# Optimization experiments

Hardware: AMD Instinct MI355X
Metric: run time of the kernel (lower is better)

## Reference

```python
import jax, jax.numpy as jnp
import numpy as np

N = 100000
E = 1600000
F_IN = 128
HID = 64


def setup_inputs() -> dict:
    key = jax.random.key(0)
    ks = jax.random.split(key, 8)
    x = jax.random.normal(ks[0], (N, F_IN), dtype=jnp.float32)
    edge_index = jax.random.randint(ks[1], (2, E), 0, N, dtype=jnp.int32)
    # GCNConv params: weight [in, out] (glorot-ish scale), bias [out]
    W1 = jax.random.normal(ks[2], (F_IN, HID), dtype=jnp.float32) / np.sqrt(F_IN)
    b1 = jnp.zeros((HID,), dtype=jnp.float32)
    W2 = jax.random.normal(ks[3], (HID, HID), dtype=jnp.float32) / np.sqrt(HID)
    b2 = jnp.zeros((HID,), dtype=jnp.float32)
    Wc = jax.random.normal(ks[4], (HID, 1), dtype=jnp.float32) / np.sqrt(HID)
    bc = jnp.zeros((1,), dtype=jnp.float32)
    return {"x": x, "edge_index": edge_index, "W1": W1, "b1": b1,
            "W2": W2, "b2": b2, "Wc": Wc, "bc": bc}


def _gcn_conv(x, src, dst, W, b):
    # PyG GCNConv: h = x @ W, then symmetric-normalized aggregation over
    # edges with self-loops: out[d] = sum_e deg^-1/2[s] deg^-1/2[d] h[s] + b
    n = x.shape[0]
    h = x @ W                                            # [N, out]
    deg = jax.ops.segment_sum(jnp.ones_like(dst, dtype=h.dtype), dst,
                              num_segments=n)            # in-degree incl. self-loops
    dinv = jnp.where(deg > 0, jax.lax.rsqrt(deg), 0.0)   # [N]
    norm = dinv[src] * dinv[dst]                         # [E+N]
    msg = h[src] * norm[:, None]                         # gather + scale
    out = jax.ops.segment_sum(msg, dst, num_segments=n)  # scatter-add
    return out + b


def reference(x, edge_index, W1, b1, W2, b2, Wc, bc):
    n = x.shape[0]
    loop = jnp.arange(n, dtype=edge_index.dtype)
    src = jnp.concatenate([edge_index[0], loop])  # add self-loops
    dst = jnp.concatenate([edge_index[1], loop])
    h = jax.nn.relu(_gcn_conv(x, src, dst, W1, b1))  # dropout in eval mode = identity
    h = jax.nn.relu(_gcn_conv(h, src, dst, W2, b2))
    return (h @ Wc + bc).squeeze(-1)  # [N]
```

## Files before the change

### kernel.cpp

```cpp
#include <hip/hip_runtime.h>


#define FIN 128
#define HIDDEN 64
#define BUCK_SH 7
#define BUCK_MASK 127
#define NBUCK 782
#define CAP 2432
#define EPB 2048

typedef __attribute__((ext_vector_type(8))) short bf16x8;
typedef __attribute__((ext_vector_type(4))) float f32x4;

__device__ __forceinline__ unsigned f2bf_pair(float a, float b) {
    unsigned ua = __float_as_uint(a);
    unsigned ub = __float_as_uint(b);
    ua = (ua + 0x7FFFu + ((ua >> 16) & 1u)) >> 16;
    ub = (ub + 0x7FFFu + ((ub >> 16) & 1u)) & 0xFFFF0000u;
    return ua | ub;
}
__device__ __forceinline__ unsigned short f2bf1(float a) {
    unsigned u = __float_as_uint(a);
    return (unsigned short)((u + 0x7FFFu + ((u >> 16) & 1u)) >> 16);
}
#define BF_LO(u) __uint_as_float((u) << 16)
#define BF_HI(u) __uint_as_float((u) & 0xFFFF0000u)

__global__ __launch_bounds__(256) void k_prep(const float* __restrict__ w1,
                                              const float* __restrict__ w2,
                                              unsigned short* __restrict__ w1t,
                                              unsigned short* __restrict__ w2t,
                                              int* __restrict__ bcursor) {
    int t = blockIdx.x * 256 + threadIdx.x;
    if (t < NBUCK) bcursor[t] = 0;
    for (int i = t; i < 64 * FIN; i += 16384) {
        int ch = i >> 7, k = i & 127;
        w1t[i] = f2bf1(w1[k * 64 + ch]);
    }
    if (t < 64 * 64) {
        int ch = t >> 6, k = t & 63;
        w2t[t] = f2bf1(w2[k * 64 + ch]);
    }
}

__global__ __launch_bounds__(256) void k_scatter_mfma1(const int* __restrict__ src,
                                                       const int* __restrict__ dst,
                                                       int* __restrict__ bcursor,
                                                       int* __restrict__ pairs, int e,
                                                       const float4* __restrict__ x4,
                                                       const unsigned short* __restrict__ w1t,
                                                       uint2* __restrict__ hsb,
                                                       int n, int nsc, int ngm) {
    __shared__ int sbuf[4352];
    int tid = threadIdx.x;
    int bid = blockIdx.x;
    bool is_sc = (bid & 1) == 0;
    int id = bid >> 1;
    if (is_sc) {
        if (id >= nsc) return;
        int* h      = sbuf;
        int* base_s = sbuf + NBUCK;
        int* cur    = sbuf + 2 * NBUCK;
        int dloc[EPB / 256];
        for (int i = tid; i < NBUCK; i += 256) { h[i] = 0; cur[i] = 0; }
        __syncthreads();
        int start = id * EPB;
#pragma unroll
        for (int i = 0; i < EPB / 256; i++) {
            int idx = start + tid + i * 256;
            int d = (idx < e) ? dst[idx] : -1;
            dloc[i] = d;
            if (d >= 0) atomicAdd(&h[d >> BUCK_SH], 1);
        }
        __syncthreads();
        for (int i = tid; i < NBUCK; i += 256)
            if (h[i] > 0) base_s[i] = atomicAdd(&bcursor[i], h[i]);
        __syncthreads();
#pragma unroll
        for (int i = 0; i < EPB / 256; i++) {
            int idx = start + tid + i * 256;
            int d = dloc[i];
            if (d >= 0) {
                int b = d >> BUCK_SH;
                int pos = base_s[b] + atomicAdd(&cur[b], 1);
                if (pos < CAP) pairs[b * CAP + pos] = (src[idx] << BUCK_SH) | (d & BUCK_MASK);
            }
        }
        return;
    }
    if (id >= ngm) return;
    unsigned short* sW = (unsigned short*)sbuf;
    {
        int ch = tid >> 2, k0 = (tid & 3) * 32;
        const uint4* g = (const uint4*)(w1t + ch * 128 + k0);
        uint4* dsd = (uint4*)(sW + ch * 136 + k0);
        uint4 a = g[0], b = g[1], c = g[2], d = g[3];
        dsd[0] = a; dsd[1] = b; dsd[2] = c; dsd[3] = d;
    }
    __syncthreads();
    int lane = tid & 63, wave = tid >> 6;
    int quad = lane >> 4, nl = lane & 15;
    const bf16x8* sW8 = (const bf16x8*)sW;
    int node0g = id * 128;
#pragma unroll
    for (int hf = 0; hf < 2; hf++) {
        int node = node0g + hf * 64 + wave * 16 + nl;
        int ic = min(node, n - 1);
        const float4* px = x4 + (size_t)ic * 32 + quad * 2;
        bf16x8 bfr[4];
#pragma unroll
        for (int kc = 0; kc < 4; kc++) {
            float4 p = px[kc * 8];
            float4 q = px[kc * 8 + 1];
            union { unsigned u[4]; bf16x8 v; } t;
            t.u[0] = f2bf_pair(p.x, p.y); t.u[1] = f2bf_pair(p.z, p.w);
            t.u[2] = f2bf_pair(q.x, q.y); t.u[3] = f2bf_pair(q.z, q.w);
            bfr[kc] = t.v;
        }
        f32x4 a0 = {0.f, 0.f, 0.f, 0.f}, a1 = a0, a2 = a0, a3 = a0;
#pragma unroll
        for (int kc = 0; kc < 4; kc++) {
            int ko = kc * 4 + quad;
            bf16x8 w0  = sW8[(nl +  0) * 17 + ko];
            bf16x8 w1f = sW8[(nl + 16) * 17 + ko];
            bf16x8 w2f = sW8[(nl + 32) * 17 + ko];
            bf16x8 w3f = sW8[(nl + 48) * 17 + ko];
            a0 = __builtin_amdgcn_mfma_f32_16x16x32_bf16(w0,  bfr[kc], a0, 0, 0, 0);
            a1 = __builtin_amdgcn_mfma_f32_16x16x32_bf16(w1f, bfr[kc], a1, 0, 0, 0);
            a2 = __builtin_amdgcn_mfma_f32_16x16x32_bf16(w2f, bfr[kc], a2, 0, 0, 0);
            a3 = __builtin_amdgcn_mfma_f32_16x16x32_bf16(w3f, bfr[kc], a3, 0, 0, 0);
        }
        if (node < n) {
            uint2* o = hsb + (size_t)node * 16 + quad;
            o[0]  = make_uint2(f2bf_pair(a0.x, a0.y), f2bf_pair(a0.z, a0.w));
            o[4]  = make_uint2(f2bf_pair(a1.x, a1.y), f2bf_pair(a1.z, a1.w));
            o[8]  = make_uint2(f2bf_pair(a2.x, a2.y), f2bf_pair(a2.z, a2.w));
            o[12] = make_uint2(f2bf_pair(a3.x, a3.y), f2bf_pair(a3.z, a3.w));
        }
    }
}

__global__ __launch_bounds__(256) void k_count(const int* __restrict__ pairs,
                                               const int* __restrict__ bcursor,
                                               float* __restrict__ dinv, int n) {
    __shared__ int cnt[128];
    int tid = threadIdx.x, b = blockIdx.x;
    if (tid < 128) cnt[tid] = 0;
    __syncthreads();
    int c = min(bcursor[b], CAP);
    const int* pb = pairs + b * CAP;
    for (int i = tid; i < c; i += 256) atomicAdd(&cnt[pb[i] & BUCK_MASK], 1);
    __syncthreads();
    int node = (b << BUCK_SH) + tid;
    if (tid < 128 && node < n) dinv[node] = rsqrtf((float)cnt[tid] + 1.0f);
}

__global__ __launch_bounds__(256) void k_agg1_gemm2(const int* __restrict__ pairs,
                                                    const int* __restrict__ bcursor,
                                                    const float* __restrict__ dinv,
                                                    const uint4* __restrict__ hsb4,
                                                    const float4* __restrict__ b1_4,
                                                    const unsigned short* __restrict__ w2t,
                                                    uint2* __restrict__ hsb2, int n) {
    __shared__ int csr_l[CAP];
    __shared__ unsigned short sW[64 * 72];
    __shared__ float sV[32 * 68];
    __shared__ int cnt[128], off_s[128], wsum[128];
    int tid = threadIdx.x, b = blockIdx.x;
    int node0 = b << BUCK_SH;
    if (tid < 128) {
        int ch = tid >> 1, k0 = (tid & 1) * 32;
        const uint4* g = (const uint4*)(w2t + ch * 64 + k0);
        uint4* dsd = (uint4*)(sW + ch * 72 + k0);
        uint4 a = g[0], bb = g[1], c = g[2], d = g[3];
        dsd[0] = a; dsd[1] = bb; dsd[2] = c; dsd[3] = d;
    } else {
        cnt[tid - 128] = 0;
    }
    __syncthreads();
    int c = min(bcursor[b], CAP);
    const int* pb = pairs + b * CAP;
    for (int i = tid; i < c; i += 256) atomicAdd(&cnt[pb[i] & BUCK_MASK], 1);
    __syncthreads();
    if (tid < 128) wsum[tid] = cnt[tid];
    __syncthreads();
    for (int o = 1; o < 128; o <<= 1) {
        int x = 0;
        if (tid < 128 && tid >= o) x = wsum[tid - o];
        __syncthreads();
        if (tid < 128 && tid >= o) wsum[tid] += x;
        __syncthreads();
    }
    if (tid < 128) { off_s[tid] = wsum[tid] - cnt[tid]; cnt[tid] = 0; }
    __syncthreads();
    for (int i = tid; i < c; i += 256) {
        int p = pb[i];
        int l = p & BUCK_MASK;
        int pos = off_s[l] + atomicAdd(&cnt[l], 1);
        csr_l[pos] = p >> BUCK_SH;
    }
    __syncthreads();
    int nloc = tid >> 3, cq = tid & 7;
    int lane = tid & 63, wave = tid >> 6;
    int quad = lane >> 4, nl = lane & 15;
    const bf16x8* sW8 = (const bf16x8*)sW;
#pragma unroll 1
    for (int ck = 0; ck < 4; ck++) {
        int loc = ck * 32 + nloc;
        int node = node0 + loc;
        int dg = cnt[loc], st = off_s[loc];
        float sd = rsqrtf((float)dg + 1.0f);
        float4 accA = make_float4(0.f, 0.f, 0.f, 0.f), accB = accA;
        if (node < n) {
            int end = st + dg;
            int nr = (dg + 3) >> 2;
            for (int r = 0; r < nr; r++) {
                int base = st + (r << 2);
                int e0 = base, e1 = base + 1, e2 = base + 2, e3 = base + 3;
                int s0 = csr_l[min(e0, end - 1)];
                int s1 = csr_l[min(e1, end - 1)];
                int s2 = csr_l[min(e2, end - 1)];
                int s3 = csr_l[min(e3, end - 1)];
                float m0 = (e0 < end) ? dinv[s0] : 0.f;
                float m1 = (e1 < end) ? dinv[s1] : 0.f;
                float m2 = (e2 < end) ? dinv[s2] : 0.f;
                float m3 = (e3 < end) ? dinv[s3] : 0.f;
                uint4 g0 = hsb4[(size_t)s0 * 8 + cq];
                uint4 g1 = hsb4[(size_t)s1 * 8 + cq];
                uint4 g2 = hsb4[(size_t)s2 * 8 + cq];
                uint4 g3 = hsb4[(size_t)s3 * 8 + cq];
                accA.x += m0 * BF_LO(g0.x) + m1 * BF_LO(g1.x) + m2 * BF_LO(g2.x) + m3 * BF_LO(g3.x);
                accA.y += m0 * BF_HI(g0.x) + m1 * BF_HI(g1.x) + m2 * BF_HI(g2.x) + m3 * BF_HI(g3.x);
                accA.z += m0 * BF_LO(g0.y) + m1 * BF_LO(g1.y) + m2 * BF_LO(g2.y) + m3 * BF_LO(g3.y);
                accA.w += m0 * BF_HI(g0.y) + m1 * BF_HI(g1.y) + m2 * BF_HI(g2.y) + m3 * BF_HI(g3.y);
                accB.x += m0 * BF_LO(g0.z) + m1 * BF_LO(g1.z) + m2 * BF_LO(g2.z) + m3 * BF_LO(g3.z);
                accB.y += m0 * BF_HI(g0.z) + m1 * BF_HI(g1.z) + m2 * BF_HI(g2.z) + m3 * BF_HI(g3.z);
                accB.z += m0 * BF_LO(g0.w) + m1 * BF_LO(g1.w) + m2 * BF_LO(g2.w) + m3 * BF_LO(g3.w);
                accB.w += m0 * BF_HI(g0.w) + m1 * BF_HI(g1.w) + m2 * BF_HI(g2.w) + m3 * BF_HI(g3.w);
            }
        }
        float4 vA = make_float4(0.f, 0.f, 0.f, 0.f), vB = vA;
        if (node < n) {
            uint4 gs = hsb4[(size_t)node * 8 + cq];
            float sq = sd * sd;
            float4 bA = b1_4[cq * 2], bB = b1_4[cq * 2 + 1];
            vA.x = fmaxf(sd * accA.x + sq * BF_LO(gs.x) + bA.x, 0.f);
            vA.y = fmaxf(sd * accA.y + sq * BF_HI(gs.x) + bA.y, 0.f);
            vA.z = fmaxf(sd * accA.z + sq * BF_LO(gs.y) + bA.z, 0.f);
            vA.w = fmaxf(sd * accA.w + sq * BF_HI(gs.y) + bA.w, 0.f);
            vB.x = fmaxf(sd * accB.x + sq * BF_LO(gs.z) + bB.x, 0.f);
            vB.y = fmaxf(sd * accB.y + sq * BF_HI(gs.z) + bB.y, 0.f);
            vB.z = fmaxf(sd * accB.z + sq * BF_LO(gs.w) + bB.z, 0.f);
            vB.w = fmaxf(sd * accB.w + sq * BF_HI(gs.w) + bB.w, 0.f);
        }
        float* vb = sV + nloc * 68 + cq * 8;
        *(float4*)vb = vA;
        *(float4*)(vb + 4) = vB;
        __syncthreads();
#pragma unroll
        for (int tt = 0; tt < 2; tt++) {
            f32x4 acc = {0.f, 0.f, 0.f, 0.f};
#pragma unroll
            for (int kc = 0; kc < 2; kc++) {
                const float* vr = sV + (tt * 16 + nl) * 68 + kc * 32 + quad * 8;
                float4 p = *(const float4*)vr;
                float4 q = *(const float4*)(vr + 4);
                union { unsigned u[4]; bf16x8 v; } t;
                t.u[0] = f2bf_pair(p.x, p.y); t.u[1] = f2bf_pair(p.z, p.w);
                t.u[2] = f2bf_pair(q.x, q.y); t.u[3] = f2bf_pair(q.z, q.w);
                bf16x8 a = sW8[(wave * 16 + nl) * 9 + kc * 4 + quad];
                acc = __builtin_amdgcn_mfma_f32_16x16x32_bf16(a, t.v, acc, 0, 0, 0);
            }
            int oloc = ck * 32 + tt * 16 + nl;
            int onode = node0 + oloc;
            if (onode < n) {
                float s = rsqrtf((float)cnt[oloc] + 1.0f);
                hsb2[(size_t)onode * 16 + wave * 4 + quad] =
                    make_uint2(f2bf_pair(acc.x * s, acc.y * s), f2bf_pair(acc.z * s, acc.w * s));
            }
        }
        __syncthreads();
    }
}

__global__ __launch_bounds__(256) void k_agg2_head(const int* __restrict__ pairs,
                                                   const int* __restrict__ bcursor,
                                                   const uint4* __restrict__ hsb4,
                                                   const float4* __restrict__ b2_4,
                                                   const float4* __restrict__ wc_4,
                                                   const float* __restrict__ bc,
                                                   float* __restrict__ out, int n) {
    __shared__ int csr_l[CAP];
    __shared__ int cnt[128], off_s[128], wsum[128];
    int tid = threadIdx.x, b = blockIdx.x;
    int node0 = b << BUCK_SH;
    if (tid < 128) cnt[tid] = 0;
    __syncthreads();
    int c = min(bcursor[b], CAP);
    const int* pb = pairs + b * CAP;
    for (int i = tid; i < c; i += 256) atomicAdd(&cnt[pb[i] & BUCK_MASK], 1);
    __syncthreads();
    if (tid < 128) wsum[tid] = cnt[tid];
    __syncthreads();
    for (int o = 1; o < 128; o <<= 1) {
        int x = 0;
        if (tid < 128 && tid >= o) x = wsum[tid - o];
        __syncthreads();
        if (tid < 128 && tid >= o) wsum[tid] += x;
        __syncthreads();
    }
    if (tid < 128) { off_s[tid] = wsum[tid] - cnt[tid]; cnt[tid] = 0; }
    __syncthreads();
    for (int i = tid; i < c; i += 256) {
        int p = pb[i];
        int l = p & BUCK_MASK;
        int pos = off_s[l] + atomicAdd(&cnt[l], 1);
        csr_l[pos] = p >> BUCK_SH;
    }
    __syncthreads();
    int nloc = tid >> 3, cq = tid & 7;
#pragma unroll 1
    for (int ck = 0; ck < 4; ck++) {
        int loc = ck * 32 + nloc;
        int node = node0 + loc;
        if (node >= n) continue;
        int dg = cnt[loc], st = off_s[loc];
        int end = st + dg;
        float4 accA = make_float4(0.f, 0.f, 0.f, 0.f), accB = accA;
        int nr = (dg + 3) >> 2;
        for (int r = 0; r < nr; r++) {
            int base = st + (r << 2);
            int e0 = base, e1 = base + 1, e2 = base + 2, e3 = base + 3;
            int s0 = csr_l[min(e0, end - 1)];
            int s1 = csr_l[min(e1, end - 1)];
            int s2 = csr_l[min(e2, end - 1)];
            int s3 = csr_l[min(e3, end - 1)];
            float m0 = (e0 < end) ? 1.f : 0.f;
            float m1 = (e1 < end) ? 1.f : 0.f;
            float m2 = (e2 < end) ? 1.f : 0.f;
            float m3 = (e3 < end) ? 1.f : 0.f;
            uint4 g0 = hsb4[(size_t)s0 * 8 + cq];
            uint4 g1 = hsb4[(size_t)s1 * 8 + cq];
            uint4 g2 = hsb4[(size_t)s2 * 8 + cq];
            uint4 g3 = hsb4[(size_t)s3 * 8 + cq];
            accA.x += m0 * BF_LO(g0.x) + m1 * BF_LO(g1.x) + m2 * BF_LO(g2.x) + m3 * BF_LO(g3.x);
            accA.y += m0 * BF_HI(g0.x) + m1 * BF_HI(g1.x) + m2 * BF_HI(g2.x) + m3 * BF_HI(g3.x);
            accA.z += m0 * BF_LO(g0.y) + m1 * BF_LO(g1.y) + m2 * BF_LO(g2.y) + m3 * BF_LO(g3.y);
            accA.w += m0 * BF_HI(g0.y) + m1 * BF_HI(g1.y) + m2 * BF_HI(g2.y) + m3 * BF_HI(g3.y);
            accB.x += m0 * BF_LO(g0.z) + m1 * BF_LO(g1.z) + m2 * BF_LO(g2.z) + m3 * BF_LO(g3.z);
            accB.y += m0 * BF_HI(g0.z) + m1 * BF_HI(g1.z) + m2 * BF_HI(g2.z) + m3 * BF_HI(g3.z);
            accB.z += m0 * BF_LO(g0.w) + m1 * BF_LO(g1.w) + m2 * BF_LO(g2.w) + m3 * BF_LO(g3.w);
            accB.w += m0 * BF_HI(g0.w) + m1 * BF_HI(g1.w) + m2 * BF_HI(g2.w) + m3 * BF_HI(g3.w);
        }
        uint4 g = hsb4[(size_t)node * 8 + cq];
        float s = rsqrtf((float)dg + 1.0f);
        float4 bA = b2_4[cq * 2], bB = b2_4[cq * 2 + 1];
        float4 wA = wc_4[cq * 2], wB = wc_4[cq * 2 + 1];
        float t = fmaxf(s * (accA.x + BF_LO(g.x)) + bA.x, 0.f) * wA.x
                + fmaxf(s * (accA.y + BF_HI(g.x)) + bA.y, 0.f) * wA.y
                + fmaxf(s * (accA.z + BF_LO(g.y)) + bA.z, 0.f) * wA.z
                + fmaxf(s * (accA.w + BF_HI(g.y)) + bA.w, 0.f) * wA.w
                + fmaxf(s * (accB.x + BF_LO(g.z)) + bB.x, 0.f) * wB.x
                + fmaxf(s * (accB.y + BF_HI(g.z)) + bB.y, 0.f) * wB.y
                + fmaxf(s * (accB.z + BF_LO(g.w)) + bB.z, 0.f) * wB.z
                + fmaxf(s * (accB.w + BF_HI(g.w)) + bB.w, 0.f) * wB.w;
        t += __shfl_xor(t, 1);
        t += __shfl_xor(t, 2);
        t += __shfl_xor(t, 4);
        if (cq == 0) out[node] = t + bc[0];
    }
}

extern "C" void kernel_launch(void* const* d_in, const int* in_sizes, int n_in,
                              void* d_out, int out_size, void* d_ws, size_t ws_size,
                              hipStream_t stream) {
    const float* x  = (const float*)d_in[0];
    const int*   ei = (const int*)d_in[1];
    const float* W1 = (const float*)d_in[2];
    const float* b1 = (const float*)d_in[3];
    const float* W2 = (const float*)d_in[4];
    const float* b2 = (const float*)d_in[5];
    const float* Wc = (const float*)d_in[6];
    const float* bc = (const float*)d_in[7];
    int n = in_sizes[0] / FIN;
    int e = in_sizes[1] / 2;
    const int* srcv = ei;
    const int* dstv = ei + e;

    char* ws = (char*)d_ws;
    float* dinv    = (float*)(ws + 0);
    int*   bcursor = (int*)(ws + (512u << 10));
    unsigned short* w1t = (unsigned short*)(ws + (528u << 10));
    unsigned short* w2t = (unsigned short*)(ws + (548u << 10));
    int*   pairs   = (int*)(ws + (1u << 20));
    uint2* hsb1    = (uint2*)(ws + (9u << 20));
    uint2* hsb2    = (uint2*)(ws + (22u << 20));

    int nb_sc   = (e + EPB - 1) / EPB;
    int nb_rows = (n + 127) / 128;
    int nb_max  = max(nb_sc, nb_rows);

    k_prep<<<64, 256, 0, stream>>>(W1, W2, w1t, w2t, bcursor);
    k_scatter_mfma1<<<2 * nb_max, 256, 0, stream>>>(srcv, dstv, bcursor, pairs, e,
                                                    (const float4*)x, w1t, hsb1,
                                                    n, nb_sc, nb_rows);
    k_count<<<NBUCK, 256, 0, stream>>>(pairs, bcursor, dinv, n);
    k_agg1_gemm2<<<NBUCK, 256, 0, stream>>>(pairs, bcursor, dinv, (const uint4*)hsb1,
                                            (const float4*)b1, w2t, hsb2, n);
    k_agg2_head<<<NBUCK, 256, 0, stream>>>(pairs, bcursor, (const uint4*)hsb2,
                                           (const float4*)b2, (const float4*)Wc,
                                           bc, (float*)d_out, n);
}
```

Baseline: 218.2 us.

## Fuse all GCN stages into one persistent cooperative kernel with grid syncs

Replaces the five separate kernel launches with a single persistent cooperative kernel of fixed grid size that walks through the phases (prep, edge scatter plus first GEMM, degree count, layer-1 aggregation plus second GEMM, layer-2 aggregation plus head) separated by grid-wide syncs. Blocks loop over work items in each phase. The edges per scatter block are doubled. The aim is to remove launch gaps and tail effects between stages. The trade-off is grid-sync cost and lower parallelism per phase with 1024 persistent blocks. If the cooperative launch fails, it falls back to five phase-specific launches.

```diff
diff --git a/kernel.cpp b/kernel.cpp
--- a/kernel.cpp
+++ b/kernel.cpp
@@ -1,13 +1,15 @@
 #include <hip/hip_runtime.h>
+#include <hip/hip_cooperative_groups.h>
+namespace cg = cooperative_groups;
 
 
 #define FIN 128
-#define HIDDEN 64
 #define BUCK_SH 7
 #define BUCK_MASK 127
 #define NBUCK 782
 #define CAP 2432
-#define EPB 2048
+#define EPB 4096
+#define GRID_BLKS 1024
 
 typedef __attribute__((ext_vector_type(8))) short bf16x8;
 typedef __attribute__((ext_vector_type(4))) float f32x4;
@@ -26,348 +28,351 @@
 #define BF_LO(u) __uint_as_float((u) << 16)
 #define BF_HI(u) __uint_as_float((u) & 0xFFFF0000u)
 
-__global__ __launch_bounds__(256) void k_prep(const float* __restrict__ w1,
-                                              const float* __restrict__ w2,
-                                              unsigned short* __restrict__ w1t,
-                                              unsigned short* __restrict__ w2t,
-                                              int* __restrict__ bcursor) {
-    int t = blockIdx.x * 256 + threadIdx.x;
-    if (t < NBUCK) bcursor[t] = 0;
-    for (int i = t; i < 64 * FIN; i += 16384) {
-        int ch = i >> 7, k = i & 127;
-        w1t[i] = f2bf1(w1[k * 64 + ch]);
-    }
-    if (t < 64 * 64) {
-        int ch = t >> 6, k = t & 63;
-        w2t[t] = f2bf1(w2[k * 64 + ch]);
-    }
-}
-
-__global__ __launch_bounds__(256) void k_scatter_mfma1(const int* __restrict__ src,
-                                                       const int* __restrict__ dst,
-                                                       int* __restrict__ bcursor,
-                                                       int* __restrict__ pairs, int e,
-                                                       const float4* __restrict__ x4,
-                                                       const unsigned short* __restrict__ w1t,
-                                                       uint2* __restrict__ hsb,
-                                                       int n, int nsc, int ngm) {
-    __shared__ int sbuf[4352];
+__global__ __launch_bounds__(256, 4) void k_gcn(
+    const int* __restrict__ src, const int* __restrict__ dst,
+    const float4* __restrict__ x4,
+    const float* __restrict__ w1, const float* __restrict__ w2,
+    const float4* __restrict__ b1_4, const float4* __restrict__ b2_4,
+    const float4* __restrict__ wc_4, const float* __restrict__ bc,
+    int* __restrict__ bcursor, int* __restrict__ pairs,
+    float* __restrict__ dinv,
+    unsigned short* __restrict__ w1t, unsigned short* __restrict__ w2t,
+    uint2* __restrict__ hsb1, uint2* __restrict__ hsb2,
+    float* __restrict__ out,
+    int n, int e, int nsc, int ngm, int phase)
+{
+    cg::grid_group grid = cg::this_grid();
+    __shared__ int smem[7296];
+    const bool all = phase < 0;
     int tid = threadIdx.x;
-    int bid = blockIdx.x;
-    bool is_sc = (bid & 1) == 0;
-    int id = bid >> 1;
-    if (is_sc) {
-        if (id >= nsc) return;
-        int* h      = sbuf;
-        int* base_s = sbuf + NBUCK;
-        int* cur    = sbuf + 2 * NBUCK;
-        int dloc[EPB / 256];
-        for (int i = tid; i < NBUCK; i += 256) { h[i] = 0; cur[i] = 0; }
-        __syncthreads();
-        int start = id * EPB;
-#pragma unroll
-        for (int i = 0; i < EPB / 256; i++) {
-            int idx = start + tid + i * 256;
-            int d = (idx < e) ? dst[idx] : -1;
-            dloc[i] = d;
-            if (d >= 0) atomicAdd(&h[d >> BUCK_SH], 1);
-        }
-        __syncthreads();
-        for (int i = tid; i < NBUCK; i += 256)
-            if (h[i] > 0) base_s[i] = atomicAdd(&bcursor[i], h[i]);
-        __syncthreads();
-#pragma unroll
-        for (int i = 0; i < EPB / 256; i++) {
-            int idx = start + tid + i * 256;
-            int d = dloc[i];
-            if (d >= 0) {
-                int b = d >> BUCK_SH;
-                int pos = base_s[b] + atomicAdd(&cur[b], 1);
-                if (pos < CAP) pairs[b * CAP + pos] = (src[idx] << BUCK_SH) | (d & BUCK_MASK);
-            }
-        }
-        return;
-    }
-    if (id >= ngm) return;
-    unsigned short* sW = (unsigned short*)sbuf;
-    {
-        int ch = tid >> 2, k0 = (tid & 3) * 32;
-        const uint4* g = (const uint4*)(w1t + ch * 128 + k0);
-        uint4* dsd = (uint4*)(sW + ch * 136 + k0);
-        uint4 a = g[0], b = g[1], c = g[2], d = g[3];
-        dsd[0] = a; dsd[1] = b; dsd[2] = c; dsd[3] = d;
-    }
-    __syncthreads();
     int lane = tid & 63, wave = tid >> 6;
     int quad = lane >> 4, nl = lane & 15;
-    const bf16x8* sW8 = (const bf16x8*)sW;
-    int node0g = id * 128;
-#pragma unroll
-    for (int hf = 0; hf < 2; hf++) {
-        int node = node0g + hf * 64 + wave * 16 + nl;
-        int ic = min(node, n - 1);
-        const float4* px = x4 + (size_t)ic * 32 + quad * 2;
-        bf16x8 bfr[4];
-#pragma unroll
-        for (int kc = 0; kc < 4; kc++) {
-            float4 p = px[kc * 8];
-            float4 q = px[kc * 8 + 1];
-            union { unsigned u[4]; bf16x8 v; } t;
-            t.u[0] = f2bf_pair(p.x, p.y); t.u[1] = f2bf_pair(p.z, p.w);
-            t.u[2] = f2bf_pair(q.x, q.y); t.u[3] = f2bf_pair(q.z, q.w);
-            bfr[kc] = t.v;
-        }
-        f32x4 a0 = {0.f, 0.f, 0.f, 0.f}, a1 = a0, a2 = a0, a3 = a0;
-#pragma unroll
-        for (int kc = 0; kc < 4; kc++) {
-            int ko = kc * 4 + quad;
-            bf16x8 w0  = sW8[(nl +  0) * 17 + ko];
-            bf16x8 w1f = sW8[(nl + 16) * 17 + ko];
-            bf16x8 w2f = sW8[(nl + 32) * 17 + ko];
-            bf16x8 w3f = sW8[(nl + 48) * 17 + ko];
-            a0 = __builtin_amdgcn_mfma_f32_16x16x32_bf16(w0,  bfr[kc], a0, 0, 0, 0);
-            a1 = __builtin_amdgcn_mfma_f32_16x16x32_bf16(w1f, bfr[kc], a1, 0, 0, 0);
-            a2 = __builtin_amdgcn_mfma_f32_16x16x32_bf16(w2f, bfr[kc], a2, 0, 0, 0);
-            a3 = __builtin_amdgcn_mfma_f32_16x16x32_bf16(w3f, bfr[kc], a3, 0, 0, 0);
-        }
-        if (node < n) {
-            uint2* o = hsb + (size_t)node * 16 + quad;
-            o[0]  = make_uint2(f2bf_pair(a0.x, a0.y), f2bf_pair(a0.z, a0.w));
-            o[4]  = make_uint2(f2bf_pair(a1.x, a1.y), f2bf_pair(a1.z, a1.w));
-            o[8]  = make_uint2(f2bf_pair(a2.x, a2.y), f2bf_pair(a2.z, a2.w));
-            o[12] = make_uint2(f2bf_pair(a3.x, a3.y), f2bf_pair(a3.z, a3.w));
-        }
-    }
-}
-
-__global__ __launch_bounds__(256) void k_count(const int* __restrict__ pairs,
-                                               const int* __restrict__ bcursor,
-                                               float* __restrict__ dinv, int n) {
-    __shared__ int cnt[128];
-    int tid = threadIdx.x, b = blockIdx.x;
-    if (tid < 128) cnt[tid] = 0;
-    __syncthreads();
-    int c = min(bcursor[b], CAP);
-    const int* pb = pairs + b * CAP;
-    for (int i = tid; i < c; i += 256) atomicAdd(&cnt[pb[i] & BUCK_MASK], 1);
-    __syncthreads();
-    int node = (b << BUCK_SH) + tid;
-    if (tid < 128 && node < n) dinv[node] = rsqrtf((float)cnt[tid] + 1.0f);
-}
-
-__global__ __launch_bounds__(256) void k_agg1_gemm2(const int* __restrict__ pairs,
-                                                    const int* __restrict__ bcursor,
-                                                    const float* __restrict__ dinv,
-                                                    const uint4* __restrict__ hsb4,
-                                                    const float4* __restrict__ b1_4,
-                                                    const unsigned short* __restrict__ w2t,
-                                                    uint2* __restrict__ hsb2, int n) {
-    __shared__ int csr_l[CAP];
-    __shared__ unsigned short sW[64 * 72];
-    __shared__ float sV[32 * 68];
-    __shared__ int cnt[128], off_s[128], wsum[128];
-    int tid = threadIdx.x, b = blockIdx.x;
-    int node0 = b << BUCK_SH;
-    if (tid < 128) {
-        int ch = tid >> 1, k0 = (tid & 1) * 32;
-        const uint4* g = (const uint4*)(w2t + ch * 64 + k0);
-        uint4* dsd = (uint4*)(sW + ch * 72 + k0);
-        uint4 a = g[0], bb = g[1], c = g[2], d = g[3];
-        dsd[0] = a; dsd[1] = bb; dsd[2] = c; dsd[3] = d;
-    } else {
-        cnt[tid - 128] = 0;
-    }
-    __syncthreads();
-    int c = min(bcursor[b], CAP);
-    const int* pb = pairs + b * CAP;
-    for (int i = tid; i < c; i += 256) atomicAdd(&cnt[pb[i] & BUCK_MASK], 1);
-    __syncthreads();
-    if (tid < 128) wsum[tid] = cnt[tid];
-    __syncthreads();
-    for (int o = 1; o < 128; o <<= 1) {
-        int x = 0;
-        if (tid < 128 && tid >= o) x = wsum[tid - o];
+    int nloc8 = tid >> 3, cq = tid & 7;
+
+    if (all || phase == 0) {
+        int gt = blockIdx.x * 256 + tid;
+        int nth = gridDim.x * 256;
+        for (int i = gt; i < NBUCK; i += nth) bcursor[i] = 0;
+        for (int i = gt; i < 64 * FIN; i += nth) {
+            int ch = i >> 7, k = i & 127;
+            w1t[i] = f2bf1(w1[k * 64 + ch]);
+        }
+        for (int i = gt; i < 64 * 64; i += nth) {
+            int ch = i >> 6, k = i & 63;
+            w2t[i] = f2bf1(w2[k * 64 + ch]);
+        }
+    }
+    if (all) grid.sync();
+
+    if (all || phase == 1) {
+        for (int w = blockIdx.x; w < nsc + ngm; w += gridDim.x) {
+            __syncthreads();
+            if (w < nsc) {
+                int* h      = smem;
+                int* base_s = smem + NBUCK;
+                int* cur    = smem + 2 * NBUCK;
+                int dloc[EPB / 256];
+                for (int i = tid; i < NBUCK; i += 256) { h[i] = 0; cur[i] = 0; }
+                __syncthreads();
+                int start = w * EPB;
+#pragma unroll
+                for (int i = 0; i < EPB / 256; i++) {
+                    int idx = start + tid + i * 256;
+                    int d = (idx < e) ? dst[idx] : -1;
+                    dloc[i] = d;
+                    if (d >= 0) atomicAdd(&h[d >> BUCK_SH], 1);
+                }
+                __syncthreads();
+                for (int i = tid; i < NBUCK; i += 256)
+                    if (h[i] > 0) base_s[i] = atomicAdd(&bcursor[i], h[i]);
+                __syncthreads();
+#pragma unroll
+                for (int i = 0; i < EPB / 256; i++) {
+                    int idx = start + tid + i * 256;
+                    int d = dloc[i];
+                    if (d >= 0) {
+                        int bb = d >> BUCK_SH;
+                        int pos = base_s[bb] + atomicAdd(&cur[bb], 1);
+                        if (pos < CAP) pairs[bb * CAP + pos] = (src[idx] << BUCK_SH) | (d & BUCK_MASK);
+                    }
+                }
+            } else {
+                int id = w - nsc;
+                unsigned short* sW = (unsigned short*)smem;
+                {
+                    int ch = tid >> 2, k0 = (tid & 3) * 32;
+                    const uint4* g = (const uint4*)(w1t + ch * 128 + k0);
+                    uint4* dsd = (uint4*)(sW + ch * 136 + k0);
+                    uint4 a = g[0], b_ = g[1], c_ = g[2], d_ = g[3];
+                    dsd[0] = a; dsd[1] = b_; dsd[2] = c_; dsd[3] = d_;
+                }
+                __syncthreads();
+                const bf16x8* sW8 = (const bf16x8*)sW;
+                int node0g = id * 128;
+#pragma unroll
+                for (int hf = 0; hf < 2; hf++) {
+                    int node = node0g + hf * 64 + wave * 16 + nl;
+                    int ic = min(node, n - 1);
+                    const float4* px = x4 + (size_t)ic * 32 + quad * 2;
+                    bf16x8 bfr[4];
+#pragma unroll
+                    for (int kc = 0; kc < 4; kc++) {
+                        float4 p = px[kc * 8];
+                        float4 q = px[kc * 8 + 1];
+                        union { unsigned u[4]; bf16x8 v; } t;
+                        t.u[0] = f2bf_pair(p.x, p.y); t.u[1] = f2bf_pair(p.z, p.w);
+                        t.u[2] = f2bf_pair(q.x, q.y); t.u[3] = f2bf_pair(q.z, q.w);
+                        bfr[kc] = t.v;
+                    }
+                    f32x4 a0 = {0.f, 0.f, 0.f, 0.f}, a1 = a0, a2 = a0, a3 = a0;
+#pragma unroll
+                    for (int kc = 0; kc < 4; kc++) {
+                        int ko = kc * 4 + quad;
+                        bf16x8 w0  = sW8[(nl +  0) * 17 + ko];
+                        bf16x8 w1f = sW8[(nl + 16) * 17 + ko];
+                        bf16x8 w2f = sW8[(nl + 32) * 17 + ko];
+                        bf16x8 w3f = sW8[(nl + 48) * 17 + ko];
+                        a0 = __builtin_amdgcn_mfma_f32_16x16x32_bf16(w0,  bfr[kc], a0, 0, 0, 0);
+                        a1 = __builtin_amdgcn_mfma_f32_16x16x32_bf16(w1f, bfr[kc], a1, 0, 0, 0);
+                        a2 = __builtin_amdgcn_mfma_f32_16x16x32_bf16(w2f, bfr[kc], a2, 0, 0, 0);
+                        a3 = __builtin_amdgcn_mfma_f32_16x16x32_bf16(w3f, bfr[kc], a3, 0, 0, 0);
+                    }
+                    if (node < n) {
+                        uint2* o = hsb1 + (size_t)node * 16 + quad;
+                        o[0]  = make_uint2(f2bf_pair(a0.x, a0.y), f2bf_pair(a0.z, a0.w));
+                        o[4]  = make_uint2(f2bf_pair(a1.x, a1.y), f2bf_pair(a1.z, a1.w));
+                        o[8]  = make_uint2(f2bf_pair(a2.x, a2.y), f2bf_pair(a2.z, a2.w));
+                        o[12] = make_uint2(f2bf_pair(a3.x, a3.y), f2bf_pair(a3.z, a3.w));
+                    }
+                }
+            }
+        }
+    }
+    if (all) grid.sync();
+
+    if (all || phase == 2) {
+        int* cnt = smem;
+        for (int b = blockIdx.x; b < NBUCK; b += gridDim.x) {
+            __syncthreads();
+            if (tid < 128) cnt[tid] = 0;
+            __syncthreads();
+            int c = min(bcursor[b], CAP);
+            const int* pb = pairs + b * CAP;
+            for (int i = tid; i < c; i += 256) atomicAdd(&cnt[pb[i] & BUCK_MASK], 1);
+            __syncthreads();
+            int node = (b << BUCK_SH) + tid;
+            if (tid < 128 && node < n) dinv[node] = rsqrtf((float)cnt[tid] + 1.0f);
+        }
+    }
+    if (all) grid.sync();
+
+    if (all || phase == 3) {
+        int* csr_l = smem;
+        unsigned short* sWp = (unsigned short*)(smem + 2432);
+        float* sV = (float*)(smem + 4736);
+        int* cnt = smem + 6912;
+        int* off_s = smem + 7040;
+        int* wsum = smem + 7168;
+        const uint4* H = (const uint4*)hsb1;
         __syncthreads();
-        if (tid < 128 && tid >= o) wsum[tid] += x;
-        __syncthreads();
-    }
-    if (tid < 128) { off_s[tid] = wsum[tid] - cnt[tid]; cnt[tid] = 0; }
-    __syncthreads();
-    for (int i = tid; i < c; i += 256) {
-        int p = pb[i];
-        int l = p & BUCK_MASK;
-        int pos = off_s[l] + atomicAdd(&cnt[l], 1);
-        csr_l[pos] = p >> BUCK_SH;
-    }
-    __syncthreads();
-    int nloc = tid >> 3, cq = tid & 7;
-    int lane = tid & 63, wave = tid >> 6;
-    int quad = lane >> 4, nl = lane & 15;
-    const bf16x8* sW8 = (const bf16x8*)sW;
-#pragma unroll 1
-    for (int ck = 0; ck < 4; ck++) {
-        int loc = ck * 32 + nloc;
-        int node = node0 + loc;
-        int dg = cnt[loc], st = off_s[loc];
-        float sd = rsqrtf((float)dg + 1.0f);
-        float4 accA = make_float4(0.f, 0.f, 0.f, 0.f), accB = accA;
-        if (node < n) {
-            int end = st + dg;
-            int nr = (dg + 3) >> 2;
-            for (int r = 0; r < nr; r++) {
-                int base = st + (r << 2);
-                int e0 = base, e1 = base + 1, e2 = base + 2, e3 = base + 3;
-                int s0 = csr_l[min(e0, end - 1)];
-                int s1 = csr_l[min(e1, end - 1)];
-                int s2 = csr_l[min(e2, end - 1)];
-                int s3 = csr_l[min(e3, end - 1)];
-                float m0 = (e0 < end) ? dinv[s0] : 0.f;
-                float m1 = (e1 < end) ? dinv[s1] : 0.f;
-                float m2 = (e2 < end) ? dinv[s2] : 0.f;
-                float m3 = (e3 < end) ? dinv[s3] : 0.f;
-                uint4 g0 = hsb4[(size_t)s0 * 8 + cq];
-                uint4 g1 = hsb4[(size_t)s1 * 8 + cq];
-                uint4 g2 = hsb4[(size_t)s2 * 8 + cq];
-                uint4 g3 = hsb4[(size_t)s3 * 8 + cq];
-                accA.x += m0 * BF_LO(g0.x) + m1 * BF_LO(g1.x) + m2 * BF_LO(g2.x) + m3 * BF_LO(g3.x);
-                accA.y += m0 * BF_HI(g0.x) + m1 * BF_HI(g1.x) + m2 * BF_HI(g2.x) + m3 * BF_HI(g3.x);
-                accA.z += m0 * BF_LO(g0.y) + m1 * BF_LO(g1.y) + m2 * BF_LO(g2.y) + m3 * BF_LO(g3.y);
-                accA.w += m0 * BF_HI(g0.y) + m1 * BF_HI(g1.y) + m2 * BF_HI(g2.y) + m3 * BF_HI(g3.y);
-                accB.x += m0 * BF_LO(g0.z) + m1 * BF_LO(g1.z) + m2 * BF_LO(g2.z) + m3 * BF_LO(g3.z);
-                accB.y += m0 * BF_HI(g0.z) + m1 * BF_HI(g1.z) + m2 * BF_HI(g2.z) + m3 * BF_HI(g3.z);
-                accB.z += m0 * BF_LO(g0.w) + m1 * BF_LO(g1.w) + m2 * BF_LO(g2.w) + m3 * BF_LO(g3.w);
-                accB.w += m0 * BF_HI(g0.w) + m1 * BF_HI(g1.w) + m2 * BF_HI(g2.w) + m3 * BF_HI(g3.w);
-            }
-        }
-        float4 vA = make_float4(0.f, 0.f, 0.f, 0.f), vB = vA;
-        if (node < n) {
-            uint4 gs = hsb4[(size_t)node * 8 + cq];
-            float sq = sd * sd;
-            float4 bA = b1_4[cq * 2], bB = b1_4[cq * 2 + 1];
-            vA.x = fmaxf(sd * accA.x + sq * BF_LO(gs.x) + bA.x, 0.f);
-            vA.y = fmaxf(sd * accA.y + sq * BF_HI(gs.x) + bA.y, 0.f);
-            vA.z = fmaxf(sd * accA.z + sq * BF_LO(gs.y) + bA.z, 0.f);
-            vA.w = fmaxf(sd * accA.w + sq * BF_HI(gs.y) + bA.w, 0.f);
-            vB.x = fmaxf(sd * accB.x + sq * BF_LO(gs.z) + bB.x, 0.f);
-            vB.y = fmaxf(sd * accB.y + sq * BF_HI(gs.z) + bB.y, 0.f);
-            vB.z = fmaxf(sd * accB.z + sq * BF_LO(gs.w) + bB.z, 0.f);
-            vB.w = fmaxf(sd * accB.w + sq * BF_HI(gs.w) + bB.w, 0.f);
-        }
-        float* vb = sV + nloc * 68 + cq * 8;
-        *(float4*)vb = vA;
-        *(float4*)(vb + 4) = vB;
-        __syncthreads();
-#pragma unroll
-        for (int tt = 0; tt < 2; tt++) {
-            f32x4 acc = {0.f, 0.f, 0.f, 0.f};
-#pragma unroll
-            for (int kc = 0; kc < 2; kc++) {
-                const float* vr = sV + (tt * 16 + nl) * 68 + kc * 32 + quad * 8;
-                float4 p = *(const float4*)vr;
-                float4 q = *(const float4*)(vr + 4);
-                union { unsigned u[4]; bf16x8 v; } t;
-                t.u[0] = f2bf_pair(p.x, p.y); t.u[1] = f2bf_pair(p.z, p.w);
-                t.u[2] = f2bf_pair(q.x, q.y); t.u[3] = f2bf_pair(q.z, q.w);
-                bf16x8 a = sW8[(wave * 16 + nl) * 9 + kc * 4 + quad];
-                acc = __builtin_amdgcn_mfma_f32_16x16x32_bf16(a, t.v, acc, 0, 0, 0);
-            }
-            int oloc = ck * 32 + tt * 16 + nl;
-            int onode = node0 + oloc;
-            if (onode < n) {
-                float s = rsqrtf((float)cnt[oloc] + 1.0f);
-                hsb2[(size_t)onode * 16 + wave * 4 + quad] =
-                    make_uint2(f2bf_pair(acc.x * s, acc.y * s), f2bf_pair(acc.z * s, acc.w * s));
-            }
-        }
-        __syncthreads();
-    }
-}
-
-__global__ __launch_bounds__(256) void k_agg2_head(const int* __restrict__ pairs,
-                                                   const int* __restrict__ bcursor,
-                                                   const uint4* __restrict__ hsb4,
-                                                   const float4* __restrict__ b2_4,
-                                                   const float4* __restrict__ wc_4,
-                                                   const float* __restrict__ bc,
-                                                   float* __restrict__ out, int n) {
-    __shared__ int csr_l[CAP];
-    __shared__ int cnt[128], off_s[128], wsum[128];
-    int tid = threadIdx.x, b = blockIdx.x;
-    int node0 = b << BUCK_SH;
-    if (tid < 128) cnt[tid] = 0;
-    __syncthreads();
-    int c = min(bcursor[b], CAP);
-    const int* pb = pairs + b * CAP;
-    for (int i = tid; i < c; i += 256) atomicAdd(&cnt[pb[i] & BUCK_MASK], 1);
-    __syncthreads();
-    if (tid < 128) wsum[tid] = cnt[tid];
-    __syncthreads();
-    for (int o = 1; o < 128; o <<= 1) {
-        int x = 0;
-        if (tid < 128 && tid >= o) x = wsum[tid - o];
-        __syncthreads();
-        if (tid < 128 && tid >= o) wsum[tid] += x;
-        __syncthreads();
-    }
-    if (tid < 128) { off_s[tid] = wsum[tid] - cnt[tid]; cnt[tid] = 0; }
-    __syncthreads();
-    for (int i = tid; i < c; i += 256) {
-        int p = pb[i];
-        int l = p & BUCK_MASK;
-        int pos = off_s[l] + atomicAdd(&cnt[l], 1);
-        csr_l[pos] = p >> BUCK_SH;
-    }
-    __syncthreads();
-    int nloc = tid >> 3, cq = tid & 7;
-#pragma unroll 1
-    for (int ck = 0; ck < 4; ck++) {
-        int loc = ck * 32 + nloc;
-        int node = node0 + loc;
-        if (node >= n) continue;
-        int dg = cnt[loc], st = off_s[loc];
-        int end = st + dg;
-        float4 accA = make_float4(0.f, 0.f, 0.f, 0.f), accB = accA;
-        int nr = (dg + 3) >> 2;
-        for (int r = 0; r < nr; r++) {
-            int base = st + (r << 2);
-            int e0 = base, e1 = base + 1, e2 = base + 2, e3 = base + 3;
-            int s0 = csr_l[min(e0, end - 1)];
-            int s1 = csr_l[min(e1, end - 1)];
-            int s2 = csr_l[min(e2, end - 1)];
-            int s3 = csr_l[min(e3, end - 1)];
-            float m0 = (e0 < end) ? 1.f : 0.f;
-            float m1 = (e1 < end) ? 1.f : 0.f;
-            float m2 = (e2 < end) ? 1.f : 0.f;
-            float m3 = (e3 < end) ? 1.f : 0.f;
-            uint4 g0 = hsb4[(size_t)s0 * 8 + cq];
-            uint4 g1 = hsb4[(size_t)s1 * 8 + cq];
-            uint4 g2 = hsb4[(size_t)s2 * 8 + cq];
-            uint4 g3 = hsb4[(size_t)s3 * 8 + cq];
-            accA.x += m0 * BF_LO(g0.x) + m1 * BF_LO(g1.x) + m2 * BF_LO(g2.x) + m3 * BF_LO(g3.x);
-            accA.y += m0 * BF_HI(g0.x) + m1 * BF_HI(g1.x) + m2 * BF_HI(g2.x) + m3 * BF_HI(g3.x);
-            accA.z += m0 * BF_LO(g0.y) + m1 * BF_LO(g1.y) + m2 * BF_LO(g2.y) + m3 * BF_LO(g3.y);
-            accA.w += m0 * BF_HI(g0.y) + m1 * BF_HI(g1.y) + m2 * BF_HI(g2.y) + m3 * BF_HI(g3.y);
-            accB.x += m0 * BF_LO(g0.z) + m1 * BF_LO(g1.z) + m2 * BF_LO(g2.z) + m3 * BF_LO(g3.z);
-            accB.y += m0 * BF_HI(g0.z) + m1 * BF_HI(g1.z) + m2 * BF_HI(g2.z) + m3 * BF_HI(g3.z);
-            accB.z += m0 * BF_LO(g0.w) + m1 * BF_LO(g1.w) + m2 * BF_LO(g2.w) + m3 * BF_LO(g3.w);
-            accB.w += m0 * BF_HI(g0.w) + m1 * BF_HI(g1.w) + m2 * BF_HI(g2.w) + m3 * BF_HI(g3.w);
-        }
-        uint4 g = hsb4[(size_t)node * 8 + cq];
-        float s = rsqrtf((float)dg + 1.0f);
-        float4 bA = b2_4[cq * 2], bB = b2_4[cq * 2 + 1];
-        float4 wA = wc_4[cq * 2], wB = wc_4[cq * 2 + 1];
-        float t = fmaxf(s * (accA.x + BF_LO(g.x)) + bA.x, 0.f) * wA.x
-                + fmaxf(s * (accA.y + BF_HI(g.x)) + bA.y, 0.f) * wA.y
-                + fmaxf(s * (accA.z + BF_LO(g.y)) + bA.z, 0.f) * wA.z
-                + fmaxf(s * (accA.w + BF_HI(g.y)) + bA.w, 0.f) * wA.w
-                + fmaxf(s * (accB.x + BF_LO(g.z)) + bB.x, 0.f) * wB.x
-                + fmaxf(s * (accB.y + BF_HI(g.z)) + bB.y, 0.f) * wB.y
-                + fmaxf(s * (accB.z + BF_LO(g.w)) + bB.z, 0.f) * wB.z
-                + fmaxf(s * (accB.w + BF_HI(g.w)) + bB.w, 0.f) * wB.w;
-        t += __shfl_xor(t, 1);
-        t += __shfl_xor(t, 2);
-        t += __shfl_xor(t, 4);
-        if (cq == 0) out[node] = t + bc[0];
+        if (tid < 128) {
+            int ch = tid >> 1, k0 = (tid & 1) * 32;
+            const uint4* g = (const uint4*)(w2t + ch * 64 + k0);
+            uint4* dsd = (uint4*)(sWp + ch * 72 + k0);
+            uint4 a = g[0], b_ = g[1], c_ = g[2], d_ = g[3];
+            dsd[0] = a; dsd[1] = b_; dsd[2] = c_; dsd[3] = d_;
+        }
+        const bf16x8* sW8 = (const bf16x8*)sWp;
+        for (int b = blockIdx.x; b < NBUCK; b += gridDim.x) {
+            __syncthreads();
+            if (tid < 128) cnt[tid] = 0;
+            __syncthreads();
+            int c = min(bcursor[b], CAP);
+            const int* pb = pairs + b * CAP;
+            for (int i = tid; i < c; i += 256) atomicAdd(&cnt[pb[i] & BUCK_MASK], 1);
+            __syncthreads();
+            if (tid < 128) wsum[tid] = cnt[tid];
+            __syncthreads();
+            for (int o = 1; o < 128; o <<= 1) {
+                int x = 0;
+                if (tid < 128 && tid >= o) x = wsum[tid - o];
+                __syncthreads();
+                if (tid < 128 && tid >= o) wsum[tid] += x;
+                __syncthreads();
+            }
+            if (tid < 128) { off_s[tid] = wsum[tid] - cnt[tid]; cnt[tid] = 0; }
+            __syncthreads();
+            for (int i = tid; i < c; i += 256) {
+                int p = pb[i];
+                int l = p & BUCK_MASK;
+                int pos = off_s[l] + atomicAdd(&cnt[l], 1);
+                csr_l[pos] = p >> BUCK_SH;
+            }
+            for (int i = c + tid; i < CAP; i += 256) csr_l[i] = 0;
+            __syncthreads();
+            int node0 = b << BUCK_SH;
+            for (int ck = 0; ck < 4; ck++) {
+                int loc = ck * 32 + nloc8;
+                int node = node0 + loc;
+                int dg = cnt[loc], st = off_s[loc];
+                float4 accA = make_float4(0.f, 0.f, 0.f, 0.f), accB = accA;
+                if (node < n) {
+                    int end = st + dg;
+                    int nr = (dg + 3) >> 2;
+                    for (int r = 0; r < nr; r++) {
+                        int base = st + (r << 2);
+                        int s0 = csr_l[max(min(base,     end - 1), 0)];
+                        int s1 = csr_l[max(min(base + 1, end - 1), 0)];
+                        int s2 = csr_l[max(min(base + 2, end - 1), 0)];
+                        int s3 = csr_l[max(min(base + 3, end - 1), 0)];
+                        float m0 = (base     < end) ? dinv[s0] : 0.f;
+                        float m1 = (base + 1 < end) ? dinv[s1] : 0.f;
+                        float m2 = (base + 2 < end) ? dinv[s2] : 0.f;
+                        float m3 = (base + 3 < end) ? dinv[s3] : 0.f;
+                        uint4 g0 = H[(size_t)s0 * 8 + cq];
+                        uint4 g1 = H[(size_t)s1 * 8 + cq];
+                        uint4 g2 = H[(size_t)s2 * 8 + cq];
+                        uint4 g3 = H[(size_t)s3 * 8 + cq];
+                        accA.x += m0 * BF_LO(g0.x) + m1 * BF_LO(g1.x) + m2 * BF_LO(g2.x) + m3 * BF_LO(g3.x);
+                        accA.y += m0 * BF_HI(g0.x) + m1 * BF_HI(g1.x) + m2 * BF_HI(g2.x) + m3 * BF_HI(g3.x);
+                        accA.z += m0 * BF_LO(g0.y) + m1 * BF_LO(g1.y) + m2 * BF_LO(g2.y) + m3 * BF_LO(g3.y);
+                        accA.w += m0 * BF_HI(g0.y) + m1 * BF_HI(g1.y) + m2 * BF_HI(g2.y) + m3 * BF_HI(g3.y);
+                        accB.x += m0 * BF_LO(g0.z) + m1 * BF_LO(g1.z) + m2 * BF_LO(g2.z) + m3 * BF_LO(g3.z);
+                        accB.y += m0 * BF_HI(g0.z) + m1 * BF_HI(g1.z) + m2 * BF_HI(g2.z) + m3 * BF_HI(g3.z);
+                        accB.z += m0 * BF_LO(g0.w) + m1 * BF_LO(g1.w) + m2 * BF_LO(g2.w) + m3 * BF_LO(g3.w);
+                        accB.w += m0 * BF_HI(g0.w) + m1 * BF_HI(g1.w) + m2 * BF_HI(g2.w) + m3 * BF_HI(g3.w);
+                    }
+                }
+                float4 vA = make_float4(0.f, 0.f, 0.f, 0.f), vB = vA;
+                if (node < n) {
+                    float sd = rsqrtf((float)dg + 1.0f);
+                    float sq = sd * sd;
+                    uint4 gs = H[(size_t)node * 8 + cq];
+                    float4 bA = b1_4[cq * 2], bB = b1_4[cq * 2 + 1];
+                    vA.x = fmaxf(sd * accA.x + sq * BF_LO(gs.x) + bA.x, 0.f);
+                    vA.y = fmaxf(sd * accA.y + sq * BF_HI(gs.x) + bA.y, 0.f);
+                    vA.z = fmaxf(sd * accA.z + sq * BF_LO(gs.y) + bA.z, 0.f);
+                    vA.w = fmaxf(sd * accA.w + sq * BF_HI(gs.y) + bA.w, 0.f);
+                    vB.x = fmaxf(sd * accB.x + sq * BF_LO(gs.z) + bB.x, 0.f);
+                    vB.y = fmaxf(sd * accB.y + sq * BF_HI(gs.z) + bB.y, 0.f);
+                    vB.z = fmaxf(sd * accB.z + sq * BF_LO(gs.w) + bB.z, 0.f);
+                    vB.w = fmaxf(sd * accB.w + sq * BF_HI(gs.w) + bB.w, 0.f);
+                }
+                float* vb = sV + nloc8 * 68 + cq * 8;
+                *(float4*)vb = vA;
+                *(float4*)(vb + 4) = vB;
+                __syncthreads();
+#pragma unroll
+                for (int tt = 0; tt < 2; tt++) {
+                    f32x4 acc = {0.f, 0.f, 0.f, 0.f};
+#pragma unroll
+                    for (int kc = 0; kc < 2; kc++) {
+                        const float* vr = sV + (tt * 16 + nl) * 68 + kc * 32 + quad * 8;
+                        float4 p = *(const float4*)vr;
+                        float4 q = *(const float4*)(vr + 4);
+                        union { unsigned u[4]; bf16x8 v; } t;
+                        t.u[0] = f2bf_pair(p.x, p.y); t.u[1] = f2bf_pair(p.z, p.w);
+                        t.u[2] = f2bf_pair(q.x, q.y); t.u[3] = f2bf_pair(q.z, q.w);
+                        bf16x8 a = sW8[(wave * 16 + nl) * 9 + kc * 4 + quad];
+                        acc = __builtin_amdgcn_mfma_f32_16x16x32_bf16(a, t.v, acc, 0, 0, 0);
+                    }
+                    int oloc = ck * 32 + tt * 16 + nl;
+                    int onode = node0 + oloc;
+                    if (onode < n) {
+                        float s = rsqrtf((float)cnt[oloc] + 1.0f);
+                        hsb2[(size_t)onode * 16 + wave * 4 + quad] =
+                            make_uint2(f2bf_pair(acc.x * s, acc.y * s), f2bf_pair(acc.z * s, acc.w * s));
+                    }
+                }
+                __syncthreads();
+            }
+        }
+    }
+    if (all) grid.sync();
+
+    if (all || phase == 4) {
+        int* csr_l = smem;
+        int* cnt = smem + 2432;
+        int* off_s = smem + 2560;
+        int* wsum = smem + 2688;
+        const uint4* H = (const uint4*)hsb2;
+        for (int b = blockIdx.x; b < NBUCK; b += gridDim.x) {
+            __syncthreads();
+            if (tid < 128) cnt[tid] = 0;
+            __syncthreads();
+            int c = min(bcursor[b], CAP);
+            const int* pb = pairs + b * CAP;
+            for (int i = tid; i < c; i += 256) atomicAdd(&cnt[pb[i] & BUCK_MASK], 1);
+            __syncthreads();
+            if (tid < 128) wsum[tid] = cnt[tid];
+            __syncthreads();
+            for (int o = 1; o < 128; o <<= 1) {
+                int x = 0;
+                if (tid < 128 && tid >= o) x = wsum[tid - o];
+                __syncthreads();
+                if (tid < 128 && tid >= o) wsum[tid] += x;
+                __syncthreads();
+            }
+            if (tid < 128) { off_s[tid] = wsum[tid] - cnt[tid]; cnt[tid] = 0; }
+            __syncthreads();
+            for (int i = tid; i < c; i += 256) {
+                int p = pb[i];
+                int l = p & BUCK_MASK;
+                int pos = off_s[l] + atomicAdd(&cnt[l], 1);
+                csr_l[pos] = p >> BUCK_SH;
+            }
+            for (int i = c + tid; i < CAP; i += 256) csr_l[i] = 0;
+            __syncthreads();
+            int node0 = b << BUCK_SH;
+            for (int ck = 0; ck < 4; ck++) {
+                int loc = ck * 32 + nloc8;
+                int node = node0 + loc;
+                if (node >= n) continue;
+                int dg = cnt[loc], st = off_s[loc];
+                int end = st + dg;
+                float4 accA = make_float4(0.f, 0.f, 0.f, 0.f), accB = accA;
+                int nr = (dg + 3) >> 2;
+                for (int r = 0; r < nr; r++) {
+                    int base = st + (r << 2);
+                    int s0 = csr_l[max(min(base,     end - 1), 0)];
+                    int s1 = csr_l[max(min(base + 1, end - 1), 0)];
+                    int s2 = csr_l[max(min(base + 2, end - 1), 0)];
+                    int s3 = csr_l[max(min(base + 3, end - 1), 0)];
+                    float m0 = (base     < end) ? 1.f : 0.f;
+                    float m1 = (base + 1 < end) ? 1.f : 0.f;
+                    float m2 = (base + 2 < end) ? 1.f : 0.f;
+                    float m3 = (base + 3 < end) ? 1.f : 0.f;
+                    uint4 g0 = H[(size_t)s0 * 8 + cq];
+                    uint4 g1 = H[(size_t)s1 * 8 + cq];
+                    uint4 g2 = H[(size_t)s2 * 8 + cq];
+                    uint4 g3 = H[(size_t)s3 * 8 + cq];
+                    accA.x += m0 * BF_LO(g0.x) + m1 * BF_LO(g1.x) + m2 * BF_LO(g2.x) + m3 * BF_LO(g3.x);
+                    accA.y += m0 * BF_HI(g0.x) + m1 * BF_HI(g1.x) + m2 * BF_HI(g2.x) + m3 * BF_HI(g3.x);
+                    accA.z += m0 * BF_LO(g0.y) + m1 * BF_LO(g1.y) + m2 * BF_LO(g2.y) + m3 * BF_LO(g3.y);
+                    accA.w += m0 * BF_HI(g0.y) + m1 * BF_HI(g1.y) + m2 * BF_HI(g2.y) + m3 * BF_HI(g3.y);
+                    accB.x += m0 * BF_LO(g0.z) + m1 * BF_LO(g1.z) + m2 * BF_LO(g2.z) + m3 * BF_LO(g3.z);
+                    accB.y += m0 * BF_HI(g0.z) + m1 * BF_HI(g1.z) + m2 * BF_HI(g2.z) + m3 * BF_HI(g3.z);
+                    accB.z += m0 * BF_LO(g0.w) + m1 * BF_LO(g1.w) + m2 * BF_LO(g2.w) + m3 * BF_LO(g3.w);
+                    accB.w += m0 * BF_HI(g0.w) + m1 * BF_HI(g1.w) + m2 * BF_HI(g2.w) + m3 * BF_HI(g3.w);
+                }
+                uint4 g = H[(size_t)node * 8 + cq];
+                float s = rsqrtf((float)dg + 1.0f);
+                float4 bA = b2_4[cq * 2], bB = b2_4[cq * 2 + 1];
+                float4 wA = wc_4[cq * 2], wB = wc_4[cq * 2 + 1];
+                float t = fmaxf(s * (accA.x + BF_LO(g.x)) + bA.x, 0.f) * wA.x
+                        + fmaxf(s * (accA.y + BF_HI(g.x)) + bA.y, 0.f) * wA.y
+                        + fmaxf(s * (accA.z + BF_LO(g.y)) + bA.z, 0.f) * wA.z
+                        + fmaxf(s * (accA.w + BF_HI(g.y)) + bA.w, 0.f) * wA.w
+                        + fmaxf(s * (accB.x + BF_LO(g.z)) + bB.x, 0.f) * wB.x
+                        + fmaxf(s * (accB.y + BF_HI(g.z)) + bB.y, 0.f) * wB.y
+                        + fmaxf(s * (accB.z + BF_LO(g.w)) + bB.z, 0.f) * wB.z
+                        + fmaxf(s * (accB.w + BF_HI(g.w)) + bB.w, 0.f) * wB.w;
+                t += __shfl_xor(t, 1);
+                t += __shfl_xor(t, 2);
+                t += __shfl_xor(t, 4);
+                if (cq == 0) out[node] = t + bc[0];
+            }
+        }
     }
 }
 
@@ -384,8 +389,13 @@
     const float* bc = (const float*)d_in[7];
     int n = in_sizes[0] / FIN;
     int e = in_sizes[1] / 2;
+
     const int* srcv = ei;
     const int* dstv = ei + e;
+    const float4* x4 = (const float4*)x;
+    const float4* b1_4 = (const float4*)b1;
+    const float4* b2_4 = (const float4*)b2;
+    const float4* wc_4 = (const float4*)Wc;
 
     char* ws = (char*)d_ws;
     float* dinv    = (float*)(ws + 0);
@@ -395,19 +405,26 @@
     int*   pairs   = (int*)(ws + (1u << 20));
     uint2* hsb1    = (uint2*)(ws + (9u << 20));
     uint2* hsb2    = (uint2*)(ws + (22u << 20));
-
-    int nb_sc   = (e + EPB - 1) / EPB;
-    int nb_rows = (n + 127) / 128;
-    int nb_max  = max(nb_sc, nb_rows);
-
-    k_prep<<<64, 256, 0, stream>>>(W1, W2, w1t, w2t, bcursor);
-    k_scatter_mfma1<<<2 * nb_max, 256, 0, stream>>>(srcv, dstv, bcursor, pairs, e,
-                                                    (const float4*)x, w1t, hsb1,
-                                                    n, nb_sc, nb_rows);
-    k_count<<<NBUCK, 256, 0, stream>>>(pairs, bcursor, dinv, n);
-    k_agg1_gemm2<<<NBUCK, 256, 0, stream>>>(pairs, bcursor, dinv, (const uint4*)hsb1,
-                                            (const float4*)b1, w2t, hsb2, n);
-    k_agg2_head<<<NBUCK, 256, 0, stream>>>(pairs, bcursor, (const uint4*)hsb2,
-                                           (const float4*)b2, (const float4*)Wc,
-                                           bc, (float*)d_out, n);
+    float* outp    = (float*)d_out;
+
+    int nsc = (e + EPB - 1) / EPB;
+    int ngm = (n + 127) / 128;
+    int phase = -1;
+
+    void* args[] = {&srcv, &dstv, &x4, &W1, &W2, &b1_4, &b2_4, &wc_4, &bc,
+                    &bcursor, &pairs, &dinv, &w1t, &w2t, &hsb1, &hsb2, &outp,
+                    &n, &e, &nsc, &ngm, &phase};
+    hipError_t err = hipLaunchCooperativeKernel((const void*)k_gcn,
+                                                dim3(GRID_BLKS), dim3(256),
+                                                args, 0, stream);
+    if (err != hipSuccess) {
+        (void)hipGetLastError();
+        for (int p = 0; p < 5; p++) {
+            k_gcn<<<GRID_BLKS, 256, 0, stream>>>(srcv, dstv, x4, W1, W2,
+                                                 b1_4, b2_4, wc_4, bc,
+                                                 bcursor, pairs, dinv, w1t, w2t,
+                                                 hsb1, hsb2, outp,
+                                                 n, e, nsc, ngm, p);
+        }
+    }
 }
```

After: 621.7 us. +184.9%, slower.
